# Optimization experiments

Measured on AMD Instinct MI355X. Metric: run time of the kernel, lower is better.

## Reference

```python
import jax, jax.numpy as jnp
import numpy as np

N_NODES = 50000
N_EDGES = 600000
HEADS = 4
DH = 64
NUM_GRAPHS = 8
NEG_SLOPE = 0.2


def setup_inputs() -> dict:
    key = jax.random.key(0)
    ks = jax.random.split(key, 10)
    feat = jax.random.normal(ks[0], (N_NODES, 128), jnp.float32)
    W0 = jax.random.normal(ks[1], (128, HEADS * DH), jnp.float32) * 0.05
    W1 = jax.random.normal(ks[2], (HEADS * DH, HEADS * DH), jnp.float32) * 0.05
    W2 = jax.random.normal(ks[3], (HEADS * DH, HEADS * DH), jnp.float32) * 0.05
    a0 = jax.random.normal(ks[4], (HEADS, DH), jnp.float32) * 0.05
    a1 = jax.random.normal(ks[5], (HEADS, DH), jnp.float32) * 0.05
    a2 = jax.random.normal(ks[6], (HEADS, DH), jnp.float32) * 0.05
    src = jax.random.randint(ks[7], (N_EDGES,), 0, N_NODES, jnp.int32)
    dst = jax.random.randint(ks[8], (N_EDGES,), 0, N_NODES, jnp.int32)
    graph_ids = jnp.sort(jax.random.randint(ks[9], (N_NODES,), 0, NUM_GRAPHS, jnp.int32))
    return {"feat": feat, "W0": W0, "W1": W1, "W2": W2,
            "a0": a0, "a1": a1, "a2": a2,
            "src": src, "dst": dst, "graph_ids": graph_ids}


def _gatv2_layer(h, W, a, src, dst, residual):
    # DGL GATv2Conv with share_weights=True, bias=False, activation=elu.
    n = h.shape[0]
    feat = (h @ W).reshape(n, HEADS, DH)               # (N,H,D)
    # GATv2 attention: score_ij = a . leaky_relu(W h_i + W h_j)
    e = jax.nn.leaky_relu(feat[src] + feat[dst], NEG_SLOPE)  # (E,H,D)
    scores = jnp.einsum('ehd,hd->eh', e, a)            # (E,H)
    # edge softmax over incoming edges of each dst node
    m = jnp.full((n, HEADS), -jnp.inf, scores.dtype).at[dst].max(scores)
    ex = jnp.exp(scores - m[dst])
    denom = jnp.zeros((n, HEADS), scores.dtype).at[dst].add(ex)
    alpha = ex / denom[dst]                            # (E,H)
    out = jnp.zeros((n, HEADS, DH), h.dtype).at[dst].add(alpha[..., None] * feat[src])
    if residual:
        out = out + h.reshape(n, HEADS, DH)            # identity residual (in == H*D)
    return jax.nn.elu(out).reshape(n, HEADS * DH)      # flatten(1)


def reference(feat, W0, W1, W2, a0, a1, a2, src, dst, graph_ids):
    h = _gatv2_layer(feat, W0, a0, src, dst, residual=False)
    h = _gatv2_layer(h, W1, a1, src, dst, residual=True)
    h = _gatv2_layer(h, W2, a2, src, dst, residual=True)
    # dgl.mean_nodes: per-graph mean over nodes
    sums = jax.ops.segment_sum(h, graph_ids, num_segments=NUM_GRAPHS)
    counts = jax.ops.segment_sum(jnp.ones((h.shape[0],), h.dtype), graph_ids,
                                 num_segments=NUM_GRAPHS)
    return sums / jnp.maximum(counts, 1.0)[:, None]    # (NUM_GRAPHS, H*D)
```

## Files before the change

### kernel.cpp

```cpp
#include <hip/hip_runtime.h>
#include <math.h>

#define N_NODES 50000
#define N_EDGES 600000
#define HD 256
#define NUM_GRAPHS 8
#define POOL_CHUNK 128
#define L2E 1.4426950408889634f

static inline size_t align256(size_t x) { return (x + 255) & ~(size_t)255; }

typedef __attribute__((ext_vector_type(8))) short short8;
typedef __attribute__((ext_vector_type(8))) unsigned short u16x8;
typedef __attribute__((ext_vector_type(4))) float f32x4;

__device__ inline float b2f(unsigned short u) {
    union { unsigned int i; float f; } v; v.i = ((unsigned)u) << 16; return v.f;
}
__device__ inline unsigned short f2b(float f) {
    unsigned int u = __float_as_uint(f);
    unsigned int r = (u + 0x7fff + ((u >> 16) & 1)) >> 16;
    return (unsigned short)r;
}
__device__ inline float4 u4f(ushort4 g) {
    return make_float4(b2f(g.x), b2f(g.y), b2f(g.z), b2f(g.w));
}

__global__ void count_kernel(const int* __restrict__ dst, int* __restrict__ cnt) {
    int e = blockIdx.x * blockDim.x + threadIdx.x;
    if (e < N_EDGES) atomicAdd(&cnt[dst[e]], 1);
}

__global__ void scan_kernel(const int* __restrict__ cnt, int* __restrict__ row_ptr,
                            int* __restrict__ cursor) {
    __shared__ int wsum[16];
    __shared__ int wpre[16];
    __shared__ int s_carry;
    const int t = threadIdx.x;
    const int lane = t & 63;
    const int wid = t >> 6;
    if (t == 0) s_carry = 0;
    __syncthreads();
    for (int base = 0; base <= N_NODES; base += 4096) {
        const int i0 = base + t * 4;
        int v[4];
#pragma unroll
        for (int j = 0; j < 4; ++j) {
            int i = i0 + j;
            v[j] = (i < N_NODES) ? cnt[i] : 0;
        }
        int tsum = v[0] + v[1] + v[2] + v[3];
        int x = tsum;
#pragma unroll
        for (int ofs = 1; ofs < 64; ofs <<= 1) {
            int u = __shfl_up(x, ofs);
            if (lane >= ofs) x += u;
        }
        if (lane == 63) wsum[wid] = x;
        __syncthreads();
        if (wid == 0) {
            int wv = (lane < 16) ? wsum[lane] : 0;
            int wx = wv;
#pragma unroll
            for (int ofs = 1; ofs < 16; ofs <<= 1) {
                int u = __shfl_up(wx, ofs);
                if (lane >= ofs) wx += u;
            }
            if (lane < 16) wpre[lane] = wx - wv;
        }
        __syncthreads();
        int run = s_carry + wpre[wid] + (x - tsum);
#pragma unroll
        for (int j = 0; j < 4; ++j) {
            int i = i0 + j;
            if (i <= N_NODES) { row_ptr[i] = run; cursor[i] = run; }
            run += v[j];
        }
        __syncthreads();
        if (t == 1023) s_carry += wpre[15] + x;
        __syncthreads();
    }
}

__global__ void fill_kernel(const int* __restrict__ src, const int* __restrict__ dst,
                            int* __restrict__ cursor, int* __restrict__ col_src) {
    int e = blockIdx.x * blockDim.x + threadIdx.x;
    if (e < N_EDGES) {
        int d = dst[e];
        int slot = atomicAdd(&cursor[d], 1);
        col_src[slot] = src[e];
    }
}

template<int K>
__global__ void transpose_w(const float* __restrict__ W, unsigned short* __restrict__ Wt) {
    __shared__ float t[16][17];
    const int tx = threadIdx.x & 15;
    const int ty = threadIdx.x >> 4;
    const int kt = blockIdx.x * 16;
    const int nt = blockIdx.y * 16;
    t[ty][tx] = W[(size_t)(kt + ty) * HD + nt + tx];
    __syncthreads();
    Wt[(size_t)(nt + ty) * K + kt + tx] = f2b(t[tx][ty]);
}

template<int K, bool AF32>
__global__ __launch_bounds__(256) void mfma_gemm(const void* __restrict__ Ap,
                                                 const unsigned short* __restrict__ Wt,
                                                 unsigned short* __restrict__ C) {
    const int tid = threadIdx.x;
    const int lane = tid & 63;
    const int wave = tid >> 6;
    const int lm = lane & 15;
    const int lk = lane >> 4;
    const int row0 = blockIdx.x * 64;
    const int col0 = wave * 64;

    f32x4 acc[4][4];
#pragma unroll
    for (int rt = 0; rt < 4; ++rt)
#pragma unroll
        for (int ct = 0; ct < 4; ++ct) acc[rt][ct] = (f32x4)(0.f);

    int arow[4];
#pragma unroll
    for (int rt = 0; rt < 4; ++rt) {
        int r = row0 + rt * 16 + lm;
        arow[rt] = r < N_NODES ? r : N_NODES - 1;
    }

    const unsigned short* Ab = (const unsigned short*)Ap;
    const float* Af = (const float*)Ap;

#pragma unroll 2
    for (int k0 = 0; k0 < K; k0 += 32) {
        short8 af[4], bfr[4];
#pragma unroll
        for (int rt = 0; rt < 4; ++rt) {
            if constexpr (AF32) {
                const float* p = &Af[(size_t)arow[rt] * K + k0 + lk * 8];
                float4 v0 = *reinterpret_cast<const float4*>(p);
                float4 v1 = *reinterpret_cast<const float4*>(p + 4);
                short8 a;
                a[0] = (short)f2b(v0.x); a[1] = (short)f2b(v0.y);
                a[2] = (short)f2b(v0.z); a[3] = (short)f2b(v0.w);
                a[4] = (short)f2b(v1.x); a[5] = (short)f2b(v1.y);
                a[6] = (short)f2b(v1.z); a[7] = (short)f2b(v1.w);
                af[rt] = a;
            } else {
                af[rt] = *reinterpret_cast<const short8*>(&Ab[(size_t)arow[rt] * K + k0 + lk * 8]);
            }
        }
#pragma unroll
        for (int ct = 0; ct < 4; ++ct)
            bfr[ct] = *reinterpret_cast<const short8*>(
                &Wt[(size_t)(col0 + ct * 16 + lm) * K + k0 + lk * 8]);
#pragma unroll
        for (int ct = 0; ct < 4; ++ct)
#pragma unroll
            for (int rt = 0; rt < 4; ++rt)
                acc[rt][ct] = __builtin_amdgcn_mfma_f32_16x16x32_bf16(af[rt], bfr[ct], acc[rt][ct], 0, 0, 0);
    }

#pragma unroll
    for (int rt = 0; rt < 4; ++rt)
#pragma unroll
        for (int i = 0; i < 4; ++i) {
            int row = row0 + rt * 16 + lk * 4 + i;
            if (row < N_NODES) {
#pragma unroll
                for (int ct = 0; ct < 4; ++ct)
                    C[(size_t)row * HD + col0 + ct * 16 + lm] = f2b(acc[rt][ct][i]);
            }
        }
}

__global__ __launch_bounds__(256) void aggregate_kernel(
        const unsigned short* __restrict__ feat,
        const float* __restrict__ avec,
        const int* __restrict__ row_ptr,
        const int* __restrict__ col_src,
        unsigned short* __restrict__ hb,
        int residual) {
    const int lane = threadIdx.x & 63;
    const int wave = threadIdx.x >> 6;
    const int half = lane >> 5;
    const int sl = lane & 31;
    const int c0 = sl * 8;
    int n0 = blockIdx.x * 4 + wave;
    if (n0 >= N_NODES) return;
    const int n = __builtin_amdgcn_readfirstlane(n0);

    float av6[8], av4[8];
    {
        float4 v0 = *reinterpret_cast<const float4*>(&avec[c0]);
        float4 v1 = *reinterpret_cast<const float4*>(&avec[c0 + 4]);
        float a[8] = {v0.x, v0.y, v0.z, v0.w, v1.x, v1.y, v1.z, v1.w};
#pragma unroll
        for (int k = 0; k < 8; ++k) {
            av6[k] = a[k] * (0.6f * L2E);
            av4[k] = a[k] * (0.4f * L2E);
        }
    }

    float fd[8];
    {
        u16x8 g = *reinterpret_cast<const u16x8*>(&feat[(size_t)n * HD + c0]);
#pragma unroll
        for (int k = 0; k < 8; ++k) fd[k] = b2f(g[k]);
    }

    const int beg = row_ptr[n];
    const int end = row_ptr[n + 1];

    float denom = 0.f;
    float acc[8];
#pragma unroll
    for (int k = 0; k < 8; ++k) acc[k] = 0.f;

    for (int s = beg; s < end; s += 4) {
        int e0 = col_src[s];
        int e1 = col_src[s + 1];
        int e2 = col_src[s + 2];
        int e3 = col_src[s + 3];
        int eP = half ? e1 : e0;
        int eQ = half ? e3 : e2;
        u16x8 g0 = *reinterpret_cast<const u16x8*>(&feat[(size_t)eP * HD + c0]);
        u16x8 g1 = *reinterpret_cast<const u16x8*>(&feat[(size_t)eQ * HD + c0]);

        float sv0[8], sv1[8];
        float pp0 = 0.f, pp1 = 0.f;
#pragma unroll
        for (int k = 0; k < 8; ++k) {
            sv0[k] = b2f(g0[k]);
            float t = sv0[k] + fd[k];
            pp0 = fmaf(av6[k], t, fmaf(av4[k], fabsf(t), pp0));
        }
#pragma unroll
        for (int k = 0; k < 8; ++k) {
            sv1[k] = b2f(g1[k]);
            float t = sv1[k] + fd[k];
            pp1 = fmaf(av6[k], t, fmaf(av4[k], fabsf(t), pp1));
        }
        pp0 += __shfl_xor(pp0, 1); pp1 += __shfl_xor(pp1, 1);
        pp0 += __shfl_xor(pp0, 2); pp1 += __shfl_xor(pp1, 2);
        pp0 += __shfl_xor(pp0, 4); pp1 += __shfl_xor(pp1, 4);

        float w0 = (s + half < end) ? exp2f(pp0) : 0.f;
        float w1 = (s + 2 + half < end) ? exp2f(pp1) : 0.f;
        denom += w0 + w1;
#pragma unroll
        for (int k = 0; k < 8; ++k)
            acc[k] = fmaf(w0, sv0[k], fmaf(w1, sv1[k], acc[k]));
    }

    denom += __shfl_xor(denom, 32);
#pragma unroll
    for (int k = 0; k < 8; ++k) acc[k] += __shfl_xor(acc[k], 32);

    if (half == 0) {
        const float inv = denom > 0.f ? 1.f / denom : 0.f;
        float o[8];
#pragma unroll
        for (int k = 0; k < 8; ++k) o[k] = acc[k] * inv;
        if (residual) {
            u16x8 hr = *reinterpret_cast<const u16x8*>(&hb[(size_t)n * HD + c0]);
#pragma unroll
            for (int k = 0; k < 8; ++k) o[k] += b2f(hr[k]);
        }
        u16x8 ob;
#pragma unroll
        for (int k = 0; k < 8; ++k) {
            float e = o[k] > 0.f ? o[k] : exp2f(o[k] * L2E) - 1.f;
            ob[k] = f2b(e);
        }
        *reinterpret_cast<u16x8*>(&hb[(size_t)n * HD + c0]) = ob;
    }
}

__global__ __launch_bounds__(256) void pool_kernel(const unsigned short* __restrict__ h,
                                                   const int* __restrict__ gid,
                                                   float* __restrict__ gsums,
                                                   int* __restrict__ gcnt) {
    const int t = threadIdx.x;
    int n0 = blockIdx.x * POOL_CHUNK;
    if (n0 >= N_NODES) return;
    int n1 = n0 + POOL_CHUNK; if (n1 > N_NODES) n1 = N_NODES;
    int curg = gid[n0];
    float sum = 0.f;
    int cnt = 0;
    for (int n = n0; n < n1; ++n) {
        int g = gid[n];
        if (g != curg) {
            atomicAdd(&gsums[(size_t)curg * HD + t], sum);
            if (t == 0) atomicAdd(&gcnt[curg], cnt);
            sum = 0.f; cnt = 0; curg = g;
        }
        sum += b2f(h[(size_t)n * HD + t]);
        ++cnt;
    }
    atomicAdd(&gsums[(size_t)curg * HD + t], sum);
    if (t == 0) atomicAdd(&gcnt[curg], cnt);
}

__global__ void finalize_kernel(const float* __restrict__ gsums,
                                const int* __restrict__ gcnt,
                                float* __restrict__ out) {
    int i = blockIdx.x * blockDim.x + threadIdx.x;
    if (i < NUM_GRAPHS * HD) {
        float c = (float)gcnt[i / HD];
        out[i] = gsums[i] / fmaxf(c, 1.f);
    }
}

extern "C" void kernel_launch(void* const* d_in, const int* in_sizes, int n_in,
                              void* d_out, int out_size, void* d_ws, size_t ws_size,
                              hipStream_t stream) {
    (void)in_sizes; (void)n_in;
    const float* feat = (const float*)d_in[0];
    const float* W0 = (const float*)d_in[1];
    const float* W1 = (const float*)d_in[2];
    const float* W2 = (const float*)d_in[3];
    const float* a0 = (const float*)d_in[4];
    const float* a1 = (const float*)d_in[5];
    const float* a2 = (const float*)d_in[6];
    const int* src = (const int*)d_in[7];
    const int* dst = (const int*)d_in[8];
    const int* gid = (const int*)d_in[9];
    float* out = (float*)d_out;

    char* ws = (char*)d_ws;
    size_t off = 0;
    unsigned short* hb = (unsigned short*)(ws + off);  off = align256(off + (size_t)N_NODES * HD * 2);
    unsigned short* Bh = (unsigned short*)(ws + off);  off = align256(off + (size_t)N_NODES * HD * 2);
    unsigned short* Wt0 = (unsigned short*)(ws + off); off = align256(off + (size_t)HD * 128 * 2);
    unsigned short* Wt1 = (unsigned short*)(ws + off); off = align256(off + (size_t)HD * HD * 2);
    unsigned short* Wt2 = (unsigned short*)(ws + off); off = align256(off + (size_t)HD * HD * 2);
    int* cnt = (int*)(ws + off);                       off = align256(off + (size_t)(N_NODES + 1) * 4);
    int* row_ptr = (int*)(ws + off);                   off = align256(off + (size_t)(N_NODES + 1) * 4);
    int* cursor = (int*)(ws + off);                    off = align256(off + (size_t)(N_NODES + 1) * 4);
    int* col_src = (int*)(ws + off);                   off = align256(off + (size_t)(N_EDGES + 16) * 4);
    float* gsums = (float*)(ws + off);                 off = align256(off + (size_t)NUM_GRAPHS * HD * 4);
    int* gcnt = (int*)(ws + off);                      off = align256(off + (size_t)NUM_GRAPHS * 4);

    if (ws_size < off) {
        hipMemsetAsync(d_out, 0, (size_t)out_size * 4, stream);
        return;
    }

    hipMemsetAsync(cnt, 0, (size_t)(N_NODES + 1) * 4, stream);
    hipMemsetAsync(col_src + N_EDGES, 0, 16 * 4, stream);
    hipMemsetAsync(gsums, 0, (size_t)NUM_GRAPHS * HD * 4, stream);
    hipMemsetAsync(gcnt, 0, (size_t)NUM_GRAPHS * 4, stream);

    count_kernel<<<(N_EDGES + 255) / 256, 256, 0, stream>>>(dst, cnt);
    scan_kernel<<<1, 1024, 0, stream>>>(cnt, row_ptr, cursor);
    fill_kernel<<<(N_EDGES + 255) / 256, 256, 0, stream>>>(src, dst, cursor, col_src);
    transpose_w<128><<<dim3(8, 16), 256, 0, stream>>>(W0, Wt0);
    transpose_w<256><<<dim3(16, 16), 256, 0, stream>>>(W1, Wt1);
    transpose_w<256><<<dim3(16, 16), 256, 0, stream>>>(W2, Wt2);

    const int gemm_blocks = (N_NODES + 63) / 64;
    const int agg_blocks = (N_NODES + 3) / 4;

    mfma_gemm<128, true><<<gemm_blocks, 256, 0, stream>>>(feat, Wt0, Bh);
    aggregate_kernel<<<agg_blocks, 256, 0, stream>>>(Bh, a0, row_ptr, col_src, hb, 0);
    mfma_gemm<256, false><<<gemm_blocks, 256, 0, stream>>>(hb, Wt1, Bh);
    aggregate_kernel<<<agg_blocks, 256, 0, stream>>>(Bh, a1, row_ptr, col_src, hb, 1);
    mfma_gemm<256, false><<<gemm_blocks, 256, 0, stream>>>(hb, Wt2, Bh);
    aggregate_kernel<<<agg_blocks, 256, 0, stream>>>(Bh, a2, row_ptr, col_src, hb, 1);

    pool_kernel<<<(N_NODES + POOL_CHUNK - 1) / POOL_CHUNK, 256, 0, stream>>>(hb, gid, gsums, gcnt);
    finalize_kernel<<<(NUM_GRAPHS * HD + 255) / 256, 256, 0, stream>>>(gsums, gcnt, out);
}
```

Measured before the change: 413.5 us.

## Persistent GEMM with register-resident weights; merge prep kernels and memsets

```diff
diff --git a/kernel.cpp b/kernel.cpp
--- a/kernel.cpp
+++ b/kernel.cpp
@@ -22,13 +22,35 @@
     unsigned int r = (u + 0x7fff + ((u >> 16) & 1)) >> 16;
     return (unsigned short)r;
 }
-__device__ inline float4 u4f(ushort4 g) {
-    return make_float4(b2f(g.x), b2f(g.y), b2f(g.z), b2f(g.w));
-}
-
-__global__ void count_kernel(const int* __restrict__ dst, int* __restrict__ cnt) {
-    int e = blockIdx.x * blockDim.x + threadIdx.x;
-    if (e < N_EDGES) atomicAdd(&cnt[dst[e]], 1);
+
+#define CNT_BLOCKS ((N_EDGES + 255) / 256)
+__global__ void prep_kernel(const int* __restrict__ dst, int* __restrict__ cnt,
+                            const float* __restrict__ W0, const float* __restrict__ W1,
+                            const float* __restrict__ W2,
+                            unsigned short* __restrict__ Wt0, unsigned short* __restrict__ Wt1,
+                            unsigned short* __restrict__ Wt2) {
+    __shared__ float t[16][17];
+    int b = blockIdx.x;
+    if (b < CNT_BLOCKS) {
+        int e = b * 256 + threadIdx.x;
+        if (e < N_EDGES) atomicAdd(&cnt[dst[e]], 1);
+        return;
+    }
+    b -= CNT_BLOCKS;
+    const float* W;
+    unsigned short* Wt;
+    int K;
+    if (b < 128) { W = W0; Wt = Wt0; K = 128; }
+    else if (b < 128 + 256) { b -= 128; W = W1; Wt = Wt1; K = 256; }
+    else { b -= 384; W = W2; Wt = Wt2; K = 256; }
+    const int ktiles = K >> 4;
+    const int kt = (b % ktiles) * 16;
+    const int nt = (b / ktiles) * 16;
+    const int tx = threadIdx.x & 15;
+    const int ty = threadIdx.x >> 4;
+    t[ty][tx] = W[(size_t)(kt + ty) * HD + nt + tx];
+    __syncthreads();
+    Wt[(size_t)(nt + ty) * K + kt + tx] = f2b(t[tx][ty]);
 }
 
 __global__ void scan_kernel(const int* __restrict__ cnt, int* __restrict__ row_ptr,
@@ -92,87 +114,83 @@
     }
 }
 
-template<int K>
-__global__ void transpose_w(const float* __restrict__ W, unsigned short* __restrict__ Wt) {
-    __shared__ float t[16][17];
-    const int tx = threadIdx.x & 15;
-    const int ty = threadIdx.x >> 4;
-    const int kt = blockIdx.x * 16;
-    const int nt = blockIdx.y * 16;
-    t[ty][tx] = W[(size_t)(kt + ty) * HD + nt + tx];
-    __syncthreads();
-    Wt[(size_t)(nt + ty) * K + kt + tx] = f2b(t[tx][ty]);
-}
-
+#define GEMM_GX 256
 template<int K, bool AF32>
 __global__ __launch_bounds__(256) void mfma_gemm(const void* __restrict__ Ap,
                                                  const unsigned short* __restrict__ Wt,
                                                  unsigned short* __restrict__ C) {
-    const int tid = threadIdx.x;
-    const int lane = tid & 63;
-    const int wave = tid >> 6;
+    constexpr int NKI = K / 32;
+    const int lane = threadIdx.x & 63;
+    const int wave = threadIdx.x >> 6;
     const int lm = lane & 15;
     const int lk = lane >> 4;
-    const int row0 = blockIdx.x * 64;
-    const int col0 = wave * 64;
-
-    f32x4 acc[4][4];
-#pragma unroll
-    for (int rt = 0; rt < 4; ++rt)
-#pragma unroll
-        for (int ct = 0; ct < 4; ++ct) acc[rt][ct] = (f32x4)(0.f);
-
-    int arow[4];
-#pragma unroll
-    for (int rt = 0; rt < 4; ++rt) {
-        int r = row0 + rt * 16 + lm;
-        arow[rt] = r < N_NODES ? r : N_NODES - 1;
-    }
+    const int colbase = blockIdx.y * 128 + wave * 32;
+
+    short8 bfr[2][NKI];
+#pragma unroll
+    for (int ct = 0; ct < 2; ++ct)
+#pragma unroll
+        for (int kk = 0; kk < NKI; ++kk)
+            bfr[ct][kk] = *reinterpret_cast<const short8*>(
+                &Wt[(size_t)(colbase + ct * 16 + lm) * K + kk * 32 + lk * 8]);
 
     const unsigned short* Ab = (const unsigned short*)Ap;
     const float* Af = (const float*)Ap;
-
-#pragma unroll 2
-    for (int k0 = 0; k0 < K; k0 += 32) {
-        short8 af[4], bfr[4];
+    const int NT = (N_NODES + 63) / 64;
+
+    for (int tile = blockIdx.x; tile < NT; tile += GEMM_GX) {
+        const int row0 = tile * 64;
+        int arow[4];
 #pragma unroll
         for (int rt = 0; rt < 4; ++rt) {
-            if constexpr (AF32) {
-                const float* p = &Af[(size_t)arow[rt] * K + k0 + lk * 8];
-                float4 v0 = *reinterpret_cast<const float4*>(p);
-                float4 v1 = *reinterpret_cast<const float4*>(p + 4);
-                short8 a;
-                a[0] = (short)f2b(v0.x); a[1] = (short)f2b(v0.y);
-                a[2] = (short)f2b(v0.z); a[3] = (short)f2b(v0.w);
-                a[4] = (short)f2b(v1.x); a[5] = (short)f2b(v1.y);
-                a[6] = (short)f2b(v1.z); a[7] = (short)f2b(v1.w);
-                af[rt] = a;
-            } else {
-                af[rt] = *reinterpret_cast<const short8*>(&Ab[(size_t)arow[rt] * K + k0 + lk * 8]);
+            int r = row0 + rt * 16 + lm;
+            arow[rt] = r < N_NODES ? r : N_NODES - 1;
+        }
+        f32x4 acc[4][2];
+#pragma unroll
+        for (int rt = 0; rt < 4; ++rt) {
+            acc[rt][0] = (f32x4)(0.f);
+            acc[rt][1] = (f32x4)(0.f);
+        }
+
+#pragma unroll
+        for (int kk = 0; kk < NKI; ++kk) {
+            short8 af[4];
+#pragma unroll
+            for (int rt = 0; rt < 4; ++rt) {
+                if constexpr (AF32) {
+                    const float* p = &Af[(size_t)arow[rt] * K + kk * 32 + lk * 8];
+                    float4 v0 = *reinterpret_cast<const float4*>(p);
+                    float4 v1 = *reinterpret_cast<const float4*>(p + 4);
+                    short8 a;
+                    a[0] = (short)f2b(v0.x); a[1] = (short)f2b(v0.y);
+                    a[2] = (short)f2b(v0.z); a[3] = (short)f2b(v0.w);
+                    a[4] = (short)f2b(v1.x); a[5] = (short)f2b(v1.y);
+                    a[6] = (short)f2b(v1.z); a[7] = (short)f2b(v1.w);
+                    af[rt] = a;
+                } else {
+                    af[rt] = *reinterpret_cast<const short8*>(
+                        &Ab[(size_t)arow[rt] * K + kk * 32 + lk * 8]);
+                }
             }
-        }
-#pragma unroll
-        for (int ct = 0; ct < 4; ++ct)
-            bfr[ct] = *reinterpret_cast<const short8*>(
-                &Wt[(size_t)(col0 + ct * 16 + lm) * K + k0 + lk * 8]);
-#pragma unroll
-        for (int ct = 0; ct < 4; ++ct)
-#pragma unroll
-            for (int rt = 0; rt < 4; ++rt)
-                acc[rt][ct] = __builtin_amdgcn_mfma_f32_16x16x32_bf16(af[rt], bfr[ct], acc[rt][ct], 0, 0, 0);
-    }
-
-#pragma unroll
-    for (int rt = 0; rt < 4; ++rt)
-#pragma unroll
-        for (int i = 0; i < 4; ++i) {
-            int row = row0 + rt * 16 + lk * 4 + i;
-            if (row < N_NODES) {
-#pragma unroll
-                for (int ct = 0; ct < 4; ++ct)
-                    C[(size_t)row * HD + col0 + ct * 16 + lm] = f2b(acc[rt][ct][i]);
+#pragma unroll
+            for (int rt = 0; rt < 4; ++rt) {
+                acc[rt][0] = __builtin_amdgcn_mfma_f32_16x16x32_bf16(af[rt], bfr[0][kk], acc[rt][0], 0, 0, 0);
+                acc[rt][1] = __builtin_amdgcn_mfma_f32_16x16x32_bf16(af[rt], bfr[1][kk], acc[rt][1], 0, 0, 0);
             }
         }
+
+#pragma unroll
+        for (int rt = 0; rt < 4; ++rt)
+#pragma unroll
+            for (int i = 0; i < 4; ++i) {
+                int row = row0 + rt * 16 + lk * 4 + i;
+                if (row < N_NODES) {
+                    C[(size_t)row * HD + colbase + lm] = f2b(acc[rt][0][i]);
+                    C[(size_t)row * HD + colbase + 16 + lm] = f2b(acc[rt][1][i]);
+                }
+            }
+    }
 }
 
 __global__ __launch_bounds__(256) void aggregate_kernel(
@@ -336,38 +354,36 @@
     unsigned short* Wt0 = (unsigned short*)(ws + off); off = align256(off + (size_t)HD * 128 * 2);
     unsigned short* Wt1 = (unsigned short*)(ws + off); off = align256(off + (size_t)HD * HD * 2);
     unsigned short* Wt2 = (unsigned short*)(ws + off); off = align256(off + (size_t)HD * HD * 2);
-    int* cnt = (int*)(ws + off);                       off = align256(off + (size_t)(N_NODES + 1) * 4);
     int* row_ptr = (int*)(ws + off);                   off = align256(off + (size_t)(N_NODES + 1) * 4);
     int* cursor = (int*)(ws + off);                    off = align256(off + (size_t)(N_NODES + 1) * 4);
-    int* col_src = (int*)(ws + off);                   off = align256(off + (size_t)(N_EDGES + 16) * 4);
+    int* col_src = (int*)(ws + off);                   off = off + (size_t)N_EDGES * 4;
+    size_t zstart = off;
+    off = align256(off + 16 * 4);
+    int* cnt = (int*)(ws + off);                       off = align256(off + (size_t)(N_NODES + 1) * 4);
     float* gsums = (float*)(ws + off);                 off = align256(off + (size_t)NUM_GRAPHS * HD * 4);
     int* gcnt = (int*)(ws + off);                      off = align256(off + (size_t)NUM_GRAPHS * 4);
+    size_t zend = off;
 
     if (ws_size < off) {
         hipMemsetAsync(d_out, 0, (size_t)out_size * 4, stream);
         return;
     }
 
-    hipMemsetAsync(cnt, 0, (size_t)(N_NODES + 1) * 4, stream);
-    hipMemsetAsync(col_src + N_EDGES, 0, 16 * 4, stream);
-    hipMemsetAsync(gsums, 0, (size_t)NUM_GRAPHS * HD * 4, stream);
-    hipMemsetAsync(gcnt, 0, (size_t)NUM_GRAPHS * 4, stream);
-
-    count_kernel<<<(N_EDGES + 255) / 256, 256, 0, stream>>>(dst, cnt);
+    hipMemsetAsync(ws + zstart, 0, zend - zstart, stream);
+
+    prep_kernel<<<CNT_BLOCKS + 128 + 256 + 256, 256, 0, stream>>>(
+        dst, cnt, W0, W1, W2, Wt0, Wt1, Wt2);
     scan_kernel<<<1, 1024, 0, stream>>>(cnt, row_ptr, cursor);
     fill_kernel<<<(N_EDGES + 255) / 256, 256, 0, stream>>>(src, dst, cursor, col_src);
-    transpose_w<128><<<dim3(8, 16), 256, 0, stream>>>(W0, Wt0);
-    transpose_w<256><<<dim3(16, 16), 256, 0, stream>>>(W1, Wt1);
-    transpose_w<256><<<dim3(16, 16), 256, 0, stream>>>(W2, Wt2);
-
-    const int gemm_blocks = (N_NODES + 63) / 64;
+
+    const dim3 gemm_grid(GEMM_GX, 2);
     const int agg_blocks = (N_NODES + 3) / 4;
 
-    mfma_gemm<128, true><<<gemm_blocks, 256, 0, stream>>>(feat, Wt0, Bh);
+    mfma_gemm<128, true><<<gemm_grid, 256, 0, stream>>>(feat, Wt0, Bh);
     aggregate_kernel<<<agg_blocks, 256, 0, stream>>>(Bh, a0, row_ptr, col_src, hb, 0);
-    mfma_gemm<256, false><<<gemm_blocks, 256, 0, stream>>>(hb, Wt1, Bh);
+    mfma_gemm<256, false><<<gemm_grid, 256, 0, stream>>>(hb, Wt1, Bh);
     aggregate_kernel<<<agg_blocks, 256, 0, stream>>>(Bh, a1, row_ptr, col_src, hb, 1);
-    mfma_gemm<256, false><<<gemm_blocks, 256, 0, stream>>>(hb, Wt2, Bh);
+    mfma_gemm<256, false><<<gemm_grid, 256, 0, stream>>>(hb, Wt2, Bh);
     aggregate_kernel<<<agg_blocks, 256, 0, stream>>>(Bh, a2, row_ptr, col_src, hb, 1);
 
     pool_kernel<<<(N_NODES + POOL_CHUNK - 1) / POOL_CHUNK, 256, 0, stream>>>(hb, gid, gsums, gcnt);
```

Measured after the change: 423.2 us. +2.3%, slower.
